# Performance work log

Hardware: AMD Instinct MI355X
Metric: run time of the kernel (lower is better)

The kernel has to match this reference:

```python
import jax, jax.numpy as jnp
import numpy as np

LOG2 = float(np.log(2.0))
CUTOFF = 10.0
INPUT_DIM = 5


def ssp(x):
    # ShiftedSoftplus
    return jax.nn.softplus(x) - LOG2


def setup_inputs() -> dict:
    key = jax.random.key(0)
    ks = jax.random.split(key, 16)
    N, E, D, G, L = 20000, 320000, 128, 100, 6
    s = 0.05
    return {
        "z": jax.random.normal(ks[0], (N, INPUT_DIM + D), jnp.float32),
        "edge_index": jax.random.randint(ks[1], (2, E), 0, N, dtype=jnp.int64),
        "edge_length": jax.random.uniform(ks[2], (E,), jnp.float32),
        "edge_attr": jax.random.uniform(ks[3], (E, G), jnp.float32),
        "emblin_w": jax.random.normal(ks[4], (D, INPUT_DIM), jnp.float32) * s,
        "emblin_b": jnp.zeros((D,), jnp.float32),
        "mlp_w1": jax.random.normal(ks[5], (L, D, G), jnp.float32) * s,
        "mlp_b1": jnp.zeros((L, D), jnp.float32),
        "mlp_w2": jax.random.normal(ks[6], (L, D, D), jnp.float32) * s,
        "mlp_b2": jnp.zeros((L, D), jnp.float32),
        "lin1_w": jax.random.normal(ks[7], (L, D, D), jnp.float32) * s,
        "lin2_w": jax.random.normal(ks[8], (L, D, D), jnp.float32) * s,
        "lin2_b": jnp.zeros((L, D), jnp.float32),
        "lin_w": jax.random.normal(ks[9], (L, D, 2 * D), jnp.float32) * s,
        "lin_b": jnp.zeros((L, D), jnp.float32),
    }


def reference(z, edge_index, edge_length, edge_attr, emblin_w, emblin_b,
              mlp_w1, mlp_b1, mlp_w2, mlp_b2, lin1_w, lin2_w, lin2_b,
              lin_w, lin_b):
    # time_emb=True path: split z into node features and time embedding
    zf, ptemb = z[:, :INPUT_DIM], z[:, INPUT_DIM:]
    h = zf @ emblin_w.T + emblin_b + ptemb          # [N, D]
    src, dst = edge_index[0], edge_index[1]
    N = h.shape[0]
    # non-smooth cutoff gate: C = (edge_length <= cutoff)
    C = (edge_length <= CUTOFF).astype(h.dtype)     # [E]
    L = mlp_w1.shape[0]
    for l in range(L):
        # edge-wise filter MLP with cutoff gate
        Wf = ssp(edge_attr @ mlp_w1[l].T + mlp_b1[l]) @ mlp_w2[l].T + mlp_b2[l]
        Wf = Wf * C[:, None]                        # [E, F]
        xf = h @ lin1_w[l].T                        # [N, F]
        m_ij = xf[src] * Wf                         # gather + elementwise, [E, F]
        m_i = jax.ops.segment_sum(m_ij, dst, num_segments=N)  # scatter-add, [N, F]
        m = ssp(m_i @ lin2_w[l].T + lin2_b[l])      # [N, D]
        h = h + (jnp.concatenate([h, m], axis=1) @ lin_w[l].T + lin_b[l])
    return h
```

## Files before the change

kernel.cpp:

```cpp
#include <hip/hip_runtime.h>

#define N_NODES 20000
#define D 128
#define E_EDGES 320000
#define G 100
#define L_LAYERS 6
#define IN_DIM 5
#define ZROW (IN_DIM + D)
#define CUTOFF_V 10.0f
#define LOG2F_ 0.69314718055994530942f

typedef __attribute__((ext_vector_type(8))) short bf16x8;
typedef __attribute__((ext_vector_type(4))) float f32x4;
typedef unsigned short ushort_t;
typedef unsigned int uint_t;

__device__ __forceinline__ float sspf(float x) {
    return fmaxf(x, 0.0f) + __logf(1.0f + __expf(-fabsf(x))) - LOG2F_;
}

__device__ __forceinline__ ushort_t f2bf(float f) {
    union { float f; uint_t u; } x; x.f = f;
    uint_t r = ((x.u >> 16) & 1u) + 0x7fffu;
    return (ushort_t)((x.u + r) >> 16);
}

__device__ __forceinline__ uint_t pack2(float a, float b) {
    return (uint_t)f2bf(a) | ((uint_t)f2bf(b) << 16);
}

__device__ __forceinline__ f32x4 mfma_bf16(bf16x8 a, bf16x8 b, f32x4 c) {
    return __builtin_amdgcn_mfma_f32_16x16x32_bf16(a, b, c, 0, 0, 0);
}

__global__ void embed_kernel(const float* __restrict__ z,
                             const float* __restrict__ ew,
                             const float* __restrict__ eb,
                             float* __restrict__ h) {
    int n = blockIdx.x;
    int d = threadIdx.x;
    const float* zr = z + (size_t)n * ZROW;
    float acc = eb[d] + zr[IN_DIM + d];
#pragma unroll
    for (int k = 0; k < IN_DIM; ++k) acc += zr[k] * ew[d * IN_DIM + k];
    h[(size_t)n * D + d] = acc;
}

__global__ void convw1_kernel(const float* __restrict__ w1, ushort_t* __restrict__ out) {
    int idx = blockIdx.x * 256 + threadIdx.x;
    int k = idx & 127;
    int nl = idx >> 7;
    out[idx] = (k < G) ? f2bf(w1[(size_t)nl * G + k]) : (ushort_t)0;
}

__global__ void castbf_kernel(const float* __restrict__ src, ushort_t* __restrict__ dst) {
    int i = blockIdx.x * 256 + threadIdx.x;
    dst[i] = f2bf(src[i]);
}

__global__ void hist_kernel(const int* __restrict__ ei, int* __restrict__ deg) {
    int e = blockIdx.x * 256 + threadIdx.x;
    atomicAdd(&deg[ei[E_EDGES + e]], 1);
}

__global__ __launch_bounds__(1024) void scan_kernel(const int* __restrict__ deg,
                                                    int* __restrict__ row_start,
                                                    int* __restrict__ cursor) {
    __shared__ int wsum[16];
    int t = threadIdx.x;
    const int CH = (N_NODES + 1023) / 1024;
    int base = t * CH;
    int s = 0;
    for (int i = 0; i < CH; ++i) {
        int idx = base + i;
        if (idx < N_NODES) s += deg[idx];
    }
    int lane = t & 63, wid = t >> 6;
    int v = s;
    for (int o = 1; o < 64; o <<= 1) {
        int u = __shfl_up(v, o, 64);
        if (lane >= o) v += u;
    }
    if (lane == 63) wsum[wid] = v;
    __syncthreads();
    if (t == 0) {
        int acc = 0;
        for (int i = 0; i < 16; ++i) { int tmp = wsum[i]; wsum[i] = acc; acc += tmp; }
    }
    __syncthreads();
    int run = v - s + wsum[wid];
    for (int i = 0; i < CH; ++i) {
        int idx = base + i;
        if (idx < N_NODES) {
            row_start[idx] = run;
            cursor[idx] = run;
            run += deg[idx];
        }
    }
    if (t == 0) row_start[N_NODES] = E_EDGES;
}

__global__ void scatter_perm_kernel(const int* __restrict__ ei, const float* __restrict__ el,
                                    int* __restrict__ cursor,
                                    int* __restrict__ perm, int* __restrict__ src_p,
                                    float* __restrict__ cm_p) {
    int e = blockIdx.x * 256 + threadIdx.x;
    int d = ei[E_EDGES + e];
    int p = atomicAdd(&cursor[d], 1);
    perm[p] = e;
    src_p[p] = ei[e];
    cm_p[p] = (el[e] <= CUTOFF_V) ? 1.0f : 0.0f;
}

__global__ void attr_perm_kernel(const float* __restrict__ edge_attr,
                                 const int* __restrict__ perm,
                                 ushort_t* __restrict__ attr_p) {
    int tid = blockIdx.x * 256 + threadIdx.x;
    int r = tid >> 5, ch = tid & 31;
    float4 v = make_float4(0.f, 0.f, 0.f, 0.f);
    if (ch < 25) {
        int pe = perm[r];
        v = *(const float4*)(edge_attr + (size_t)pe * G + ch * 4);
    }
    uint2 p; p.x = pack2(v.x, v.y); p.y = pack2(v.z, v.w);
    *(uint2*)(attr_p + (size_t)r * 128 + ch * 4) = p;
}

__global__ __launch_bounds__(128) void edge_mlp_kernel(
    const ushort_t* __restrict__ attr_p, const float* __restrict__ cm_p,
    const ushort_t* __restrict__ w1b, const float* __restrict__ b1,
    const ushort_t* __restrict__ w2b, const float* __restrict__ b2,
    ushort_t* __restrict__ wf) {
    __shared__ __align__(16) ushort_t sT[32][136];

    int t = threadIdx.x, lane = t & 63, wid = t >> 6;
    int c = lane & 15, quad = lane >> 4;
    int er0 = blockIdx.x * 32;
    int mbase = wid * 64;

    f32x4 acc[2][4];
#pragma unroll
    for (int st = 0; st < 2; ++st)
#pragma unroll
        for (int ct = 0; ct < 4; ++ct) acc[st][ct] = (f32x4){0.f, 0.f, 0.f, 0.f};

#pragma unroll
    for (int ks = 0; ks < 4; ++ks) {
        int koff = ks * 32 + quad * 8;
        bf16x8 b0  = *(const bf16x8*)(attr_p + (size_t)(er0 + c) * 128 + koff);
        bf16x8 b1v = *(const bf16x8*)(attr_p + (size_t)(er0 + 16 + c) * 128 + koff);
#pragma unroll
        for (int ct = 0; ct < 4; ++ct) {
            bf16x8 a = *(const bf16x8*)(w1b + (size_t)(mbase + ct * 16 + c) * 128 + koff);
            acc[0][ct] = mfma_bf16(a, b0, acc[0][ct]);
            acc[1][ct] = mfma_bf16(a, b1v, acc[1][ct]);
        }
    }
#pragma unroll
    for (int st = 0; st < 2; ++st)
#pragma unroll
        for (int ct = 0; ct < 4; ++ct) {
            int col = mbase + ct * 16 + quad * 4;
            float4 bv = *(const float4*)(b1 + col);
            uint2 p;
            p.x = pack2(sspf(acc[st][ct][0] + bv.x), sspf(acc[st][ct][1] + bv.y));
            p.y = pack2(sspf(acc[st][ct][2] + bv.z), sspf(acc[st][ct][3] + bv.w));
            *(uint2*)(&sT[st * 16 + c][col]) = p;
        }

    __syncthreads();

#pragma unroll
    for (int st = 0; st < 2; ++st)
#pragma unroll
        for (int ct = 0; ct < 4; ++ct) acc[st][ct] = (f32x4){0.f, 0.f, 0.f, 0.f};
#pragma unroll
    for (int ks = 0; ks < 4; ++ks) {
        int koff = ks * 32 + quad * 8;
        bf16x8 b0  = *(const bf16x8*)(&sT[c][koff]);
        bf16x8 b1v = *(const bf16x8*)(&sT[16 + c][koff]);
#pragma unroll
        for (int ct = 0; ct < 4; ++ct) {
            bf16x8 a = *(const bf16x8*)(w2b + (size_t)(mbase + ct * 16 + c) * 128 + koff);
            acc[0][ct] = mfma_bf16(a, b0, acc[0][ct]);
            acc[1][ct] = mfma_bf16(a, b1v, acc[1][ct]);
        }
    }
#pragma unroll
    for (int st = 0; st < 2; ++st) {
        int e = er0 + st * 16 + c;
        float cv = cm_p[e];
#pragma unroll
        for (int ct = 0; ct < 4; ++ct) {
            int col = mbase + ct * 16 + quad * 4;
            float4 bv = *(const float4*)(b2 + col);
            uint2 p;
            p.x = pack2((acc[st][ct][0] + bv.x) * cv, (acc[st][ct][1] + bv.y) * cv);
            p.y = pack2((acc[st][ct][2] + bv.z) * cv, (acc[st][ct][3] + bv.w) * cv);
            *(uint2*)(wf + (size_t)e * 128 + col) = p;
        }
    }
}

template <bool HASB, bool SSP, bool RES, bool BF16OUT, bool TWOK>
__global__ __launch_bounds__(128) void node_mfma_kernel(
    const float* __restrict__ in0, const float* __restrict__ in1,
    const ushort_t* __restrict__ Wb, const float* __restrict__ bias,
    const float* __restrict__ resid, void* __restrict__ outp) {
    __shared__ __align__(16) ushort_t sT[32][136];
    const int WS = TWOK ? 256 : 128;
    int t = threadIdx.x, lane = t & 63, wid = t >> 6;
    int c = lane & 15, quad = lane >> 4;
    int n0 = blockIdx.x * 32;
    int mbase = wid * 64;

    f32x4 acc[2][4];
#pragma unroll
    for (int st = 0; st < 2; ++st)
#pragma unroll
        for (int ct = 0; ct < 4; ++ct) acc[st][ct] = (f32x4){0.f, 0.f, 0.f, 0.f};

    const float* src = in0;
#pragma unroll 1
    for (int ph = 0; ph < (TWOK ? 2 : 1); ++ph) {
        if (ph) __syncthreads();
#pragma unroll
        for (int i = 0; i < 8; ++i) {
            int idx = i * 128 + t;
            int r = idx >> 5, ch = idx & 31;
            int gr = n0 + r;
            float4 v = make_float4(0.f, 0.f, 0.f, 0.f);
            if (gr < N_NODES) v = *(const float4*)(src + (size_t)gr * 128 + ch * 4);
            uint2 p; p.x = pack2(v.x, v.y); p.y = pack2(v.z, v.w);
            *(uint2*)(&sT[r][ch * 4]) = p;
        }
        __syncthreads();
        int kb = ph * 128;
#pragma unroll
        for (int ks = 0; ks < 4; ++ks) {
            int koff = ks * 32 + quad * 8;
            bf16x8 b0  = *(const bf16x8*)(&sT[c][koff]);
            bf16x8 b1v = *(const bf16x8*)(&sT[16 + c][koff]);
#pragma unroll
            for (int ct = 0; ct < 4; ++ct) {
                bf16x8 a = *(const bf16x8*)(Wb + (size_t)(mbase + ct * 16 + c) * WS + kb + koff);
                acc[0][ct] = mfma_bf16(a, b0, acc[0][ct]);
                acc[1][ct] = mfma_bf16(a, b1v, acc[1][ct]);
            }
        }
        src = in1;
    }

#pragma unroll
    for (int st = 0; st < 2; ++st) {
        int node = n0 + st * 16 + c;
        if (node < N_NODES) {
#pragma unroll
            for (int ct = 0; ct < 4; ++ct) {
                int col = mbase + ct * 16 + quad * 4;
                float4 bv = make_float4(0.f, 0.f, 0.f, 0.f);
                if (HASB) bv = *(const float4*)(bias + col);
                float v0 = acc[st][ct][0] + bv.x;
                float v1 = acc[st][ct][1] + bv.y;
                float v2 = acc[st][ct][2] + bv.z;
                float v3 = acc[st][ct][3] + bv.w;
                if (SSP) { v0 = sspf(v0); v1 = sspf(v1); v2 = sspf(v2); v3 = sspf(v3); }
                if (RES) {
                    float4 rv = *(const float4*)(resid + (size_t)node * 128 + col);
                    v0 += rv.x; v1 += rv.y; v2 += rv.z; v3 += rv.w;
                }
                if (BF16OUT) {
                    uint2 p; p.x = pack2(v0, v1); p.y = pack2(v2, v3);
                    *(uint2*)((ushort_t*)outp + (size_t)node * 128 + col) = p;
                } else {
                    *(float4*)((float*)outp + (size_t)node * 128 + col) =
                        make_float4(v0, v1, v2, v3);
                }
            }
        }
    }
}

__global__ __launch_bounds__(256) void segsum_kernel(
    const ushort_t* __restrict__ wf, const ushort_t* __restrict__ xf_bf,
    const int* __restrict__ row_start, const int* __restrict__ src_p,
    float* __restrict__ m_i) {
    int t = threadIdx.x, lane = t & 63;
    int n = blockIdx.x * 4 + (t >> 6);
    int beg = row_start[n], end = row_start[n + 1];
    float a0 = 0.f, a1 = 0.f;
    for (int i = beg; i < end; ++i) {
        uint_t w = *(const uint_t*)(wf + (size_t)i * 128 + lane * 2);
        uint_t x = *(const uint_t*)(xf_bf + (size_t)src_p[i] * 128 + lane * 2);
        a0 += __uint_as_float(w << 16) * __uint_as_float(x << 16);
        a1 += __uint_as_float(w & 0xffff0000u) * __uint_as_float(x & 0xffff0000u);
    }
    *(float2*)(m_i + (size_t)n * 128 + lane * 2) = make_float2(a0, a1);
}

extern "C" void kernel_launch(void* const* d_in, const int* in_sizes, int n_in,
                              void* d_out, int out_size, void* d_ws, size_t ws_size,
                              hipStream_t stream) {
    const float* z        = (const float*)d_in[0];
    const int*   ei       = (const int*)d_in[1];
    const float* el       = (const float*)d_in[2];
    const float* ea       = (const float*)d_in[3];
    const float* emblin_w = (const float*)d_in[4];
    const float* emblin_b = (const float*)d_in[5];
    const float* mlp_w1   = (const float*)d_in[6];
    const float* mlp_b1   = (const float*)d_in[7];
    const float* mlp_w2   = (const float*)d_in[8];
    const float* mlp_b2   = (const float*)d_in[9];
    const float* lin1_w   = (const float*)d_in[10];
    const float* lin2_w   = (const float*)d_in[11];
    const float* lin2_b   = (const float*)d_in[12];
    const float* lin_w    = (const float*)d_in[13];
    const float* lin_b    = (const float*)d_in[14];
    (void)in_sizes; (void)n_in; (void)out_size; (void)ws_size;

    const size_t ND = (size_t)N_NODES * D;
    float* ws   = (float*)d_ws;
    float* h    = ws;
    float* m_i  = h + ND;
    float* cm_p = m_i + ND;
    float* fend = cm_p + E_EDGES;

    ushort_t* w1b    = (ushort_t*)fend;
    ushort_t* w2b    = w1b   + (size_t)L_LAYERS * D * 128;
    ushort_t* lin1b  = w2b   + (size_t)L_LAYERS * D * D;
    ushort_t* lin2b  = lin1b + (size_t)L_LAYERS * D * D;
    ushort_t* linwb  = lin2b + (size_t)L_LAYERS * D * D;
    ushort_t* wf     = linwb + (size_t)L_LAYERS * D * 256;
    ushort_t* xf_bf  = wf    + (size_t)E_EDGES * 128;
    ushort_t* attr_p = xf_bf + ND;
    int* ibase      = (int*)(attr_p + (size_t)E_EDGES * 128);
    int* deg        = ibase;
    int* row_start  = deg + N_NODES;
    int* cursor     = row_start + N_NODES + 1;
    int* perm       = cursor + N_NODES;
    int* src_p      = perm + E_EDGES;

    convw1_kernel<<<(L_LAYERS * D * 128) / 256, 256, 0, stream>>>(mlp_w1, w1b);
    castbf_kernel<<<(L_LAYERS * D * D) / 256, 256, 0, stream>>>(mlp_w2, w2b);
    castbf_kernel<<<(L_LAYERS * D * D) / 256, 256, 0, stream>>>(lin1_w, lin1b);
    castbf_kernel<<<(L_LAYERS * D * D) / 256, 256, 0, stream>>>(lin2_w, lin2b);
    castbf_kernel<<<(L_LAYERS * D * 256) / 256, 256, 0, stream>>>(lin_w, linwb);

    hipMemsetAsync(deg, 0, (size_t)N_NODES * sizeof(int), stream);
    hist_kernel<<<E_EDGES / 256, 256, 0, stream>>>(ei, deg);
    scan_kernel<<<1, 1024, 0, stream>>>(deg, row_start, cursor);
    scatter_perm_kernel<<<E_EDGES / 256, 256, 0, stream>>>(ei, el, cursor, perm, src_p, cm_p);
    attr_perm_kernel<<<(E_EDGES * 32) / 256, 256, 0, stream>>>(ea, perm, attr_p);

    embed_kernel<<<N_NODES, D, 0, stream>>>(z, emblin_w, emblin_b, h);

    const int NBLK = (N_NODES + 31) / 32;
    for (int l = 0; l < L_LAYERS; ++l) {
        node_mfma_kernel<false, false, false, true, false><<<NBLK, 128, 0, stream>>>(
            h, nullptr, lin1b + (size_t)l * D * D, nullptr, nullptr, xf_bf);
        edge_mlp_kernel<<<E_EDGES / 32, 128, 0, stream>>>(
            attr_p, cm_p, w1b + (size_t)l * D * 128, mlp_b1 + (size_t)l * D,
            w2b + (size_t)l * D * D, mlp_b2 + (size_t)l * D, wf);
        segsum_kernel<<<N_NODES / 4, 256, 0, stream>>>(wf, xf_bf, row_start, src_p, m_i);
        node_mfma_kernel<true, true, false, false, false><<<NBLK, 128, 0, stream>>>(
            m_i, nullptr, lin2b + (size_t)l * D * D, lin2_b + (size_t)l * D,
            nullptr, m_i);
        node_mfma_kernel<true, false, true, false, true><<<NBLK, 128, 0, stream>>>(
            h, m_i, linwb + (size_t)l * D * 256, lin_b + (size_t)l * D, h, h);
    }

    hipMemcpyAsync(d_out, h, ND * sizeof(float), hipMemcpyDeviceToDevice, stream);
}
```

Before: 1.481 ms.

## Process multiple edge tiles per block with prefetch of next attribute tile

The edge MLP kernel now handles four 32-edge tiles per block instead of one. While the second GEMM runs, it prefetches the next tile's attribute rows into registers, hiding global load latency and amortizing block launch. The cost is more register pressure, an extra barrier per tile, and a quarter as many blocks, which lowers parallelism on a GPU with many CUs.

After: 1.644 ms. 1.11x slower.

```diff
diff --git a/kernel.cpp b/kernel.cpp
--- a/kernel.cpp
+++ b/kernel.cpp
@@ -126,6 +126,7 @@
     *(uint2*)(attr_p + (size_t)r * 128 + ch * 4) = p;
 }
 
+#define ETILES 4
 __global__ __launch_bounds__(128) void edge_mlp_kernel(
     const ushort_t* __restrict__ attr_p, const float* __restrict__ cm_p,
     const ushort_t* __restrict__ w1b, const float* __restrict__ b1,
@@ -135,69 +136,97 @@
 
     int t = threadIdx.x, lane = t & 63, wid = t >> 6;
     int c = lane & 15, quad = lane >> 4;
-    int er0 = blockIdx.x * 32;
+    int eb0 = blockIdx.x * (32 * ETILES);
     int mbase = wid * 64;
 
-    f32x4 acc[2][4];
-#pragma unroll
-    for (int st = 0; st < 2; ++st)
-#pragma unroll
-        for (int ct = 0; ct < 4; ++ct) acc[st][ct] = (f32x4){0.f, 0.f, 0.f, 0.f};
-
+    const ushort_t* arow0 = attr_p + (size_t)(eb0 + c) * 128 + quad * 8;
+    const ushort_t* arow1 = attr_p + (size_t)(eb0 + 16 + c) * 128 + quad * 8;
+
+    bf16x8 ar0[4], ar1[4];
 #pragma unroll
     for (int ks = 0; ks < 4; ++ks) {
-        int koff = ks * 32 + quad * 8;
-        bf16x8 b0  = *(const bf16x8*)(attr_p + (size_t)(er0 + c) * 128 + koff);
-        bf16x8 b1v = *(const bf16x8*)(attr_p + (size_t)(er0 + 16 + c) * 128 + koff);
-#pragma unroll
-        for (int ct = 0; ct < 4; ++ct) {
-            bf16x8 a = *(const bf16x8*)(w1b + (size_t)(mbase + ct * 16 + c) * 128 + koff);
-            acc[0][ct] = mfma_bf16(a, b0, acc[0][ct]);
-            acc[1][ct] = mfma_bf16(a, b1v, acc[1][ct]);
-        }
-    }
-#pragma unroll
-    for (int st = 0; st < 2; ++st)
-#pragma unroll
-        for (int ct = 0; ct < 4; ++ct) {
-            int col = mbase + ct * 16 + quad * 4;
-            float4 bv = *(const float4*)(b1 + col);
-            uint2 p;
-            p.x = pack2(sspf(acc[st][ct][0] + bv.x), sspf(acc[st][ct][1] + bv.y));
-            p.y = pack2(sspf(acc[st][ct][2] + bv.z), sspf(acc[st][ct][3] + bv.w));
-            *(uint2*)(&sT[st * 16 + c][col]) = p;
-        }
-
-    __syncthreads();
-
-#pragma unroll
-    for (int st = 0; st < 2; ++st)
-#pragma unroll
-        for (int ct = 0; ct < 4; ++ct) acc[st][ct] = (f32x4){0.f, 0.f, 0.f, 0.f};
-#pragma unroll
-    for (int ks = 0; ks < 4; ++ks) {
-        int koff = ks * 32 + quad * 8;
-        bf16x8 b0  = *(const bf16x8*)(&sT[c][koff]);
-        bf16x8 b1v = *(const bf16x8*)(&sT[16 + c][koff]);
-#pragma unroll
-        for (int ct = 0; ct < 4; ++ct) {
-            bf16x8 a = *(const bf16x8*)(w2b + (size_t)(mbase + ct * 16 + c) * 128 + koff);
-            acc[0][ct] = mfma_bf16(a, b0, acc[0][ct]);
-            acc[1][ct] = mfma_bf16(a, b1v, acc[1][ct]);
-        }
-    }
-#pragma unroll
-    for (int st = 0; st < 2; ++st) {
-        int e = er0 + st * 16 + c;
-        float cv = cm_p[e];
-#pragma unroll
-        for (int ct = 0; ct < 4; ++ct) {
-            int col = mbase + ct * 16 + quad * 4;
-            float4 bv = *(const float4*)(b2 + col);
-            uint2 p;
-            p.x = pack2((acc[st][ct][0] + bv.x) * cv, (acc[st][ct][1] + bv.y) * cv);
-            p.y = pack2((acc[st][ct][2] + bv.z) * cv, (acc[st][ct][3] + bv.w) * cv);
-            *(uint2*)(wf + (size_t)e * 128 + col) = p;
+        ar0[ks] = *(const bf16x8*)(arow0 + ks * 32);
+        ar1[ks] = *(const bf16x8*)(arow1 + ks * 32);
+    }
+
+#pragma unroll
+    for (int tile = 0; tile < ETILES; ++tile) {
+        f32x4 acc[2][4];
+#pragma unroll
+        for (int st = 0; st < 2; ++st)
+#pragma unroll
+            for (int ct = 0; ct < 4; ++ct) acc[st][ct] = (f32x4){0.f, 0.f, 0.f, 0.f};
+
+#pragma unroll
+        for (int ks = 0; ks < 4; ++ks) {
+            int koff = ks * 32 + quad * 8;
+#pragma unroll
+            for (int ct = 0; ct < 4; ++ct) {
+                bf16x8 a = *(const bf16x8*)(w1b + (size_t)(mbase + ct * 16 + c) * 128 + koff);
+                acc[0][ct] = mfma_bf16(a, ar0[ks], acc[0][ct]);
+                acc[1][ct] = mfma_bf16(a, ar1[ks], acc[1][ct]);
+            }
+        }
+
+        bf16x8 nx0[4], nx1[4];
+        if (tile + 1 < ETILES) {
+            size_t toff = (size_t)(tile + 1) * 32 * 128;
+#pragma unroll
+            for (int ks = 0; ks < 4; ++ks) {
+                nx0[ks] = *(const bf16x8*)(arow0 + toff + ks * 32);
+                nx1[ks] = *(const bf16x8*)(arow1 + toff + ks * 32);
+            }
+        }
+
+#pragma unroll
+        for (int st = 0; st < 2; ++st)
+#pragma unroll
+            for (int ct = 0; ct < 4; ++ct) {
+                int col = mbase + ct * 16 + quad * 4;
+                float4 bv = *(const float4*)(b1 + col);
+                uint2 p;
+                p.x = pack2(sspf(acc[st][ct][0] + bv.x), sspf(acc[st][ct][1] + bv.y));
+                p.y = pack2(sspf(acc[st][ct][2] + bv.z), sspf(acc[st][ct][3] + bv.w));
+                *(uint2*)(&sT[st * 16 + c][col]) = p;
+            }
+
+        __syncthreads();
+
+#pragma unroll
+        for (int st = 0; st < 2; ++st)
+#pragma unroll
+            for (int ct = 0; ct < 4; ++ct) acc[st][ct] = (f32x4){0.f, 0.f, 0.f, 0.f};
+#pragma unroll
+        for (int ks = 0; ks < 4; ++ks) {
+            int koff = ks * 32 + quad * 8;
+            bf16x8 b0  = *(const bf16x8*)(&sT[c][koff]);
+            bf16x8 b1v = *(const bf16x8*)(&sT[16 + c][koff]);
+#pragma unroll
+            for (int ct = 0; ct < 4; ++ct) {
+                bf16x8 a = *(const bf16x8*)(w2b + (size_t)(mbase + ct * 16 + c) * 128 + koff);
+                acc[0][ct] = mfma_bf16(a, b0, acc[0][ct]);
+                acc[1][ct] = mfma_bf16(a, b1v, acc[1][ct]);
+            }
+        }
+#pragma unroll
+        for (int st = 0; st < 2; ++st) {
+            int e = eb0 + tile * 32 + st * 16 + c;
+            float cv = cm_p[e];
+#pragma unroll
+            for (int ct = 0; ct < 4; ++ct) {
+                int col = mbase + ct * 16 + quad * 4;
+                float4 bv = *(const float4*)(b2 + col);
+                uint2 p;
+                p.x = pack2((acc[st][ct][0] + bv.x) * cv, (acc[st][ct][1] + bv.y) * cv);
+                p.y = pack2((acc[st][ct][2] + bv.z) * cv, (acc[st][ct][3] + bv.w) * cv);
+                *(uint2*)(wf + (size_t)e * 128 + col) = p;
+            }
+        }
+
+        if (tile + 1 < ETILES) {
+            __syncthreads();
+#pragma unroll
+            for (int ks = 0; ks < 4; ++ks) { ar0[ks] = nx0[ks]; ar1[ks] = nx1[ks]; }
         }
     }
 }
@@ -358,7 +387,7 @@
     for (int l = 0; l < L_LAYERS; ++l) {
         node_mfma_kernel<false, false, false, true, false><<<NBLK, 128, 0, stream>>>(
             h, nullptr, lin1b + (size_t)l * D * D, nullptr, nullptr, xf_bf);
-        edge_mlp_kernel<<<E_EDGES / 32, 128, 0, stream>>>(
+        edge_mlp_kernel<<<E_EDGES / (32 * ETILES), 128, 0, stream>>>(
             attr_p, cm_p, w1b + (size_t)l * D * 128, mlp_b1 + (size_t)l * D,
             w2b + (size_t)l * D * D, mlp_b2 + (size_t)l * D, wf);
         segsum_kernel<<<N_NODES / 4, 256, 0, stream>>>(wf, xf_bf, row_start, src_p, m_i);
```
